# Performance work log

Hardware: AMD Instinct MI355X
Metric: run time of the kernel (lower is better)

The kernel has to match this reference:

```python
import jax, jax.numpy as jnp
import numpy as np

N_NODES = 50000
N_EDGES = 800000
D_IN = 256
D_HID = 256
D_OUT = 256


def sage_conv(x, src, dst, W_l, b_l, W_r, num_nodes):
    """PyG SAGEConv with mean aggregation: lin_l(mean_{j in N(i)} x_j) + lin_r(x_i)."""
    msg = x[src]  # [E, C] gather of source-node features
    agg = jax.ops.segment_sum(msg, dst, num_segments=num_nodes)  # [N, C]
    cnt = jax.ops.segment_sum(jnp.ones((src.shape[0],), x.dtype), dst,
                              num_segments=num_nodes)
    mean = agg / jnp.maximum(cnt, 1.0)[:, None]  # isolated nodes -> 0
    return mean @ W_l.T + b_l + x @ W_r.T


def setup_inputs() -> dict:
    key = jax.random.key(0)
    ks = jax.random.split(key, 10)
    s = 1.0 / np.sqrt(D_IN)
    x = jax.random.normal(ks[0], (N_NODES, D_IN), dtype=jnp.float32)
    edge_index = jax.random.randint(ks[1], (2, N_EDGES), 0, N_NODES, dtype=jnp.int64)
    mention_index = jax.random.randint(ks[2], (1,), 0, N_NODES, dtype=jnp.int64)
    return {
        "x": x,
        "edge_index": edge_index,
        "mention_index": mention_index,
        "W1_l": jax.random.uniform(ks[3], (D_HID, D_IN), jnp.float32, -s, s),
        "b1_l": jnp.zeros((D_HID,), jnp.float32),
        "W1_r": jax.random.uniform(ks[4], (D_HID, D_IN), jnp.float32, -s, s),
        "W2_l": jax.random.uniform(ks[5], (D_OUT, D_HID), jnp.float32, -s, s),
        "b2_l": jnp.zeros((D_OUT,), jnp.float32),
        "W2_r": jax.random.uniform(ks[6], (D_OUT, D_HID), jnp.float32, -s, s),
    }


def reference(x, edge_index, mention_index, W1_l, b1_l, W1_r, W2_l, b2_l, W2_r):
    src, dst = edge_index[0], edge_index[1]
    h = jax.nn.relu(sage_conv(x, src, dst, W1_l, b1_l, W1_r, N_NODES))
    h = sage_conv(h, src, dst, W2_l, b2_l, W2_r, N_NODES)
    # dropout in the original is a no-op (result discarded)
    logits = (h[mention_index] * h).sum(axis=1)  # [N]
    z = jax.nn.softmax(logits, axis=0)
    return z
```

## Files before the change

kernel.cpp:

```cpp
#include <hip/hip_runtime.h>
#include <math.h>

#define N_NODES 50000
#define N_EDGES 800000
#define D 256
#define K2 512
#define M_PAD 50048
#define BM 128
#define BN 256
#define BK 32
#define SCAN_B 196
#define SPX_B 12500
#define SPB_B 128
#define CNT_B 3125

typedef __attribute__((ext_vector_type(8))) short short8;
typedef __attribute__((ext_vector_type(8))) unsigned short ushort8;
typedef __attribute__((ext_vector_type(4))) float floatx4;

__device__ __forceinline__ unsigned short bf16_rn(float f) {
    union { float f; unsigned u; } a; a.f = f;
    unsigned r = a.u + 0x7FFF + ((a.u >> 16) & 1);
    return (unsigned short)(r >> 16);
}
__device__ __forceinline__ float bf16_to_f(unsigned short h) {
    union { unsigned u; float f; } a; a.u = ((unsigned)h) << 16;
    return a.f;
}
__device__ __forceinline__ void load_lds16(const void* g, void* lds) {
    __builtin_amdgcn_global_load_lds((const __attribute__((address_space(1))) void*)g,
                                     (__attribute__((address_space(3))) void*)lds, 16, 0, 0);
}

__global__ __launch_bounds__(256) void k_init(const float* __restrict__ x,
                                              const float* __restrict__ Wl,
                                              const float* __restrict__ Wr,
                                              const int* __restrict__ dst,
                                              unsigned short* __restrict__ Ahi,
                                              unsigned short* __restrict__ Alo,
                                              unsigned short* __restrict__ Bhi,
                                              unsigned short* __restrict__ Blo,
                                              int* __restrict__ deg) {
    int b = blockIdx.x;
    if (b < SPX_B) {
        int t = b * 256 + threadIdx.x;
        int m = t >> 6, j = (t & 63) * 4;
        float4 v = *(const float4*)&x[(size_t)m * D + j];
        ushort4 hi, lo;
        hi.x = bf16_rn(v.x); lo.x = bf16_rn(v.x - bf16_to_f(hi.x));
        hi.y = bf16_rn(v.y); lo.y = bf16_rn(v.y - bf16_to_f(hi.y));
        hi.z = bf16_rn(v.z); lo.z = bf16_rn(v.z - bf16_to_f(hi.z));
        hi.w = bf16_rn(v.w); lo.w = bf16_rn(v.w - bf16_to_f(hi.w));
        *(ushort4*)&Ahi[(size_t)m * K2 + 256 + j] = hi;
        *(ushort4*)&Alo[(size_t)m * K2 + 256 + j] = lo;
    } else if (b < SPX_B + SPB_B) {
        int t = (b - SPX_B) * 256 + threadIdx.x;
        int n = t >> 7, k = (t & 127) * 4;
        const float* srcp = (k < 256) ? &Wl[(size_t)n * 256 + k] : &Wr[(size_t)n * 256 + k - 256];
        float4 v = *(const float4*)srcp;
        ushort4 hi, lo;
        hi.x = bf16_rn(v.x); lo.x = bf16_rn(v.x - bf16_to_f(hi.x));
        hi.y = bf16_rn(v.y); lo.y = bf16_rn(v.y - bf16_to_f(hi.y));
        hi.z = bf16_rn(v.z); lo.z = bf16_rn(v.z - bf16_to_f(hi.z));
        hi.w = bf16_rn(v.w); lo.w = bf16_rn(v.w - bf16_to_f(hi.w));
        *(ushort4*)&Bhi[(size_t)n * K2 + k] = hi;
        *(ushort4*)&Blo[(size_t)n * K2 + k] = lo;
    } else {
        int e = (b - SPX_B - SPB_B) * 256 + threadIdx.x;
        if (e < N_EDGES) atomicAdd(&deg[dst[e]], 1);
    }
}

__global__ void k_scan1(const int* __restrict__ deg, int* __restrict__ bsum) {
    __shared__ int red[256];
    int b = blockIdx.x, t = threadIdx.x;
    int i = b * 256 + t;
    red[t] = (i < N_NODES) ? deg[i] : 0;
    __syncthreads();
    for (int o = 128; o; o >>= 1) {
        if (t < o) red[t] += red[t + o];
        __syncthreads();
    }
    if (t == 0) bsum[b] = red[0];
}

__global__ void k_scan23(const int* __restrict__ deg, const int* __restrict__ bsum,
                         int* __restrict__ cursor) {
    __shared__ int sh[256];
    int b = blockIdx.x, t = threadIdx.x;
    sh[t] = (t < SCAN_B) ? bsum[t] : 0;
    __syncthreads();
    for (int o = 1; o < 256; o <<= 1) {
        int v = (t >= o) ? sh[t - o] : 0;
        __syncthreads();
        sh[t] += v;
        __syncthreads();
    }
    int boff = (b == 0) ? 0 : sh[b - 1];
    __syncthreads();
    int i = b * 256 + t;
    int v = (i < N_NODES) ? deg[i] : 0;
    sh[t] = v;
    __syncthreads();
    for (int o = 1; o < 256; o <<= 1) {
        int val = (t >= o) ? sh[t - o] : 0;
        __syncthreads();
        sh[t] += val;
        __syncthreads();
    }
    if (i < N_NODES) cursor[i] = boff + sh[t] - v;
}

__global__ void k_bucket(const int* __restrict__ src, const int* __restrict__ dst,
                         int* __restrict__ cursor, int* __restrict__ csr_src) {
    int e = blockIdx.x * blockDim.x + threadIdx.x;
    if (e >= N_EDGES) return;
    int pos = atomicAdd(&cursor[dst[e]], 1);
    csr_src[pos] = src[e];
}

__global__ __launch_bounds__(256) void k_agg(const int* __restrict__ cursor,
                                             const int* __restrict__ deg,
                                             const int* __restrict__ csr,
                                             unsigned short* __restrict__ Ahi,
                                             unsigned short* __restrict__ Alo) {
    int node = blockIdx.x * 4 + (threadIdx.x >> 6);
    int lane = threadIdx.x & 63;
    if (node >= N_NODES) return;
    int d = deg[node], end = cursor[node], start = end - d;
    int h = lane >> 5;
    int col = (lane & 31) * 8;
    const unsigned short* Xb = Ahi + 256 + col;
    float acc0[8] = {}, acc1[8] = {}, acc2[8] = {}, acc3[8] = {};
    int j = start;
    for (; j + 8 <= end; j += 8) {
        int i0 = csr[j + h], i1 = csr[j + 2 + h], i2 = csr[j + 4 + h], i3 = csr[j + 6 + h];
        ushort8 v0 = *(const ushort8*)&Xb[(size_t)i0 * K2];
        ushort8 v1 = *(const ushort8*)&Xb[(size_t)i1 * K2];
        ushort8 v2 = *(const ushort8*)&Xb[(size_t)i2 * K2];
        ushort8 v3 = *(const ushort8*)&Xb[(size_t)i3 * K2];
        #pragma unroll
        for (int k = 0; k < 8; k++) {
            acc0[k] += bf16_to_f(v0[k]);
            acc1[k] += bf16_to_f(v1[k]);
            acc2[k] += bf16_to_f(v2[k]);
            acc3[k] += bf16_to_f(v3[k]);
        }
    }
    if (j + 4 <= end) {
        int i0 = csr[j + h], i1 = csr[j + 2 + h];
        ushort8 v0 = *(const ushort8*)&Xb[(size_t)i0 * K2];
        ushort8 v1 = *(const ushort8*)&Xb[(size_t)i1 * K2];
        #pragma unroll
        for (int k = 0; k < 8; k++) {
            acc0[k] += bf16_to_f(v0[k]);
            acc1[k] += bf16_to_f(v1[k]);
        }
        j += 4;
    }
    if (j + 2 <= end) {
        int i0 = csr[j + h];
        ushort8 v0 = *(const ushort8*)&Xb[(size_t)i0 * K2];
        #pragma unroll
        for (int k = 0; k < 8; k++) acc0[k] += bf16_to_f(v0[k]);
        j += 2;
    }
    if (j < end && h == 0) {
        int i0 = csr[j];
        ushort8 v0 = *(const ushort8*)&Xb[(size_t)i0 * K2];
        #pragma unroll
        for (int k = 0; k < 8; k++) acc0[k] += bf16_to_f(v0[k]);
    }
    float inv = 1.0f / fmaxf((float)d, 1.0f);
    ushort8 hi, lo;
    #pragma unroll
    for (int k = 0; k < 8; k++) {
        float a = (acc0[k] + acc1[k]) + (acc2[k] + acc3[k]);
        a += __shfl_xor(a, 32);
        float m = a * inv;
        hi[k] = bf16_rn(m);
        lo[k] = bf16_rn(m - bf16_to_f(hi[k]));
    }
    if (h == 0) {
        *(ushort8*)&Ahi[(size_t)node * K2 + col] = hi;
        *(ushort8*)&Alo[(size_t)node * K2 + col] = lo;
    }
}

__global__ __launch_bounds__(256) void k_small(const int* __restrict__ mention,
                                               const int* __restrict__ deg,
                                               const int* __restrict__ cursor,
                                               const int* __restrict__ csr,
                                               const float* __restrict__ x,
                                               const float* __restrict__ W1l,
                                               const float* __restrict__ W1r,
                                               const float* __restrict__ b1,
                                               float* __restrict__ h1m) {
    int m = mention[0];
    int dm = min(deg[m], 95);
    int slot = blockIdx.x;
    if (slot > dm) return;
    int startm = cursor[m] - deg[m];
    int node = (slot == 0) ? m : csr[startm + slot - 1];
    __shared__ float smean[D], sx[D];
    int t = threadIdx.x;
    int d = deg[node], end = cursor[node], start = end - d;
    float a = 0.f;
    for (int j = start; j < end; j++) a += x[(size_t)csr[j] * D + t];
    smean[t] = a / fmaxf((float)d, 1.0f);
    sx[t] = x[(size_t)node * D + t];
    __syncthreads();
    float z = b1[t];
    for (int k = 0; k < D; k++)
        z += smean[k] * W1l[(size_t)t * D + k] + sx[k] * W1r[(size_t)t * D + k];
    h1m[(size_t)slot * D + t] = fmaxf(z, 0.f);
}

__global__ __launch_bounds__(256) void k_vu(const int* __restrict__ mention,
                                            const int* __restrict__ deg,
                                            const float* __restrict__ h1m,
                                            const float* __restrict__ W2l,
                                            const float* __restrict__ W2r,
                                            const float* __restrict__ b2,
                                            float* __restrict__ u,
                                            float* __restrict__ cout) {
    __shared__ float sm[D], sh[D], sv[D], red[256];
    int m = mention[0];
    int dm = min(deg[m], 95);
    int t = threadIdx.x;
    float a = 0.f;
    for (int j = 1; j <= dm; j++) a += h1m[(size_t)j * D + t];
    sm[t] = a / fmaxf((float)deg[m], 1.0f);
    sh[t] = h1m[t];
    __syncthreads();
    float acc = b2[t];
    for (int k = 0; k < D; k++)
        acc += sm[k] * W2l[(size_t)t * D + k] + sh[k] * W2r[(size_t)t * D + k];
    sv[t] = acc;
    red[t] = b2[t] * acc;
    __syncthreads();
    for (int o = 128; o; o >>= 1) {
        if (t < o) red[t] += red[t + o];
        __syncthreads();
    }
    if (t == 0) cout[0] = red[0];
    float a1 = 0.f, a2 = 0.f;
    for (int n = 0; n < D; n++) {
        a1 += W2l[(size_t)n * D + t] * sv[n];
        a2 += W2r[(size_t)n * D + t] * sv[n];
    }
    u[t] = a1;
    u[D + t] = a2;
}

__global__ __launch_bounds__(512, 4)
void k_gemm_fused(const unsigned short* __restrict__ Ahi,
                  const unsigned short* __restrict__ Alo,
                  const unsigned short* __restrict__ Bhi,
                  const unsigned short* __restrict__ Blo,
                  const float* __restrict__ bias,
                  const float* __restrict__ u,
                  float* __restrict__ s,
                  float* __restrict__ t_) {
    __shared__ unsigned short sA[2][BM * BK];
    __shared__ unsigned short sB[2][BN * BK];
    __shared__ float sred[BM], tred[BM];
    int tid = threadIdx.x;
    int br = blockIdx.x;
    int lane = tid & 63, wv = tid >> 6;
    int wm = (wv >> 2) * 64, wn = (wv & 3) * 64;
    int q = lane >> 4, r = lane & 15;

    float biasv[4], u1v[4], u2v[4];
    #pragma unroll
    for (int nt = 0; nt < 4; nt++) {
        int gc = wn + nt * 16 + r;
        biasv[nt] = bias[gc];
        u1v[nt] = u[gc];
        u2v[nt] = u[256 + gc];
    }
    if (tid < BM) { sred[tid] = 0.f; tred[tid] = 0.f; }

    floatx4 acc[4][4] = {};

    const size_t arow0 = (size_t)br * BM;
    int seg = lane & 3;
    int rl16 = lane >> 2;

    for (int kt = 0; kt < K2 / BK; kt++) {
        {
            int rloc = wv * 16 + rl16;
            size_t gA = (arow0 + rloc) * (size_t)K2 + kt * BK + seg * 8;
            int ldsoff = (wv * 16) * BK;
            load_lds16(Ahi + gA, &sA[0][ldsoff]);
            load_lds16(Alo + gA, &sA[1][ldsoff]);
        }
        #pragma unroll
        for (int t = 0; t < 2; t++) {
            int rloc = wv * 32 + t * 16 + rl16;
            size_t gB = (size_t)rloc * K2 + kt * BK + seg * 8;
            int ldsoff = (wv * 32 + t * 16) * BK;
            load_lds16(Bhi + gB, &sB[0][ldsoff]);
            load_lds16(Blo + gB, &sB[1][ldsoff]);
        }
        __syncthreads();
        short8 ah[4], al[4], bh[4], bl[4];
        #pragma unroll
        for (int i = 0; i < 4; i++) {
            ah[i] = *(const short8*)&sA[0][(wm + i * 16 + r) * BK + q * 8];
            al[i] = *(const short8*)&sA[1][(wm + i * 16 + r) * BK + q * 8];
            bh[i] = *(const short8*)&sB[0][(wn + i * 16 + r) * BK + q * 8];
            bl[i] = *(const short8*)&sB[1][(wn + i * 16 + r) * BK + q * 8];
        }
        #pragma unroll
        for (int mt = 0; mt < 4; mt++)
            #pragma unroll
            for (int nt = 0; nt < 4; nt++) {
                acc[mt][nt] = __builtin_amdgcn_mfma_f32_16x16x32_bf16(ah[mt], bh[nt], acc[mt][nt], 0, 0, 0);
                acc[mt][nt] = __builtin_amdgcn_mfma_f32_16x16x32_bf16(ah[mt], bl[nt], acc[mt][nt], 0, 0, 0);
                acc[mt][nt] = __builtin_amdgcn_mfma_f32_16x16x32_bf16(al[mt], bh[nt], acc[mt][nt], 0, 0, 0);
            }
        __syncthreads();
    }

    #pragma unroll
    for (int mt = 0; mt < 4; mt++) {
        #pragma unroll
        for (int reg = 0; reg < 4; reg++) {
            float sacc = 0.f, tacc = 0.f;
            #pragma unroll
            for (int nt = 0; nt < 4; nt++) {
                float h = fmaxf(acc[mt][nt][reg] + biasv[nt], 0.f);
                sacc += h * u1v[nt];
                tacc += h * u2v[nt];
            }
            #pragma unroll
            for (int off = 1; off < 16; off <<= 1) {
                sacc += __shfl_xor(sacc, off);
                tacc += __shfl_xor(tacc, off);
            }
            if (r == 0) {
                int row = wm + mt * 16 + q * 4 + reg;
                atomicAdd(&sred[row], sacc);
                atomicAdd(&tred[row], tacc);
            }
        }
    }
    __syncthreads();
    if (tid < BM) {
        size_t grow = arow0 + tid;
        if (grow < N_NODES) {
            s[grow] = sred[tid];
            t_[grow] = tred[tid];
        }
    }
}

__global__ __launch_bounds__(256) void k_logits_sm1(const int* __restrict__ deg,
                                                    const int* __restrict__ cursor,
                                                    const int* __restrict__ csr,
                                                    const float* __restrict__ s,
                                                    const float* __restrict__ t_,
                                                    const float* __restrict__ cptr,
                                                    float* __restrict__ logits,
                                                    float* __restrict__ pmax,
                                                    float* __restrict__ psum) {
    __shared__ float red[256];
    int b = blockIdx.x, t = threadIdx.x;
    int i = b * 256 + t;
    float lg = -INFINITY;
    if (i < N_NODES) {
        int d = deg[i];
        int end = cursor[i];
        int start = end - d;
        float sum = 0.f;
        for (int j = start; j < end; j++) sum += s[csr[j]];
        lg = sum / fmaxf((float)d, 1.0f) + t_[i] + cptr[0];
        logits[i] = lg;
    }
    red[t] = lg;
    __syncthreads();
    for (int o = 128; o; o >>= 1) {
        if (t < o) red[t] = fmaxf(red[t], red[t + o]);
        __syncthreads();
    }
    float mb = red[0];
    __syncthreads();
    red[t] = (i < N_NODES) ? __expf(lg - mb) : 0.f;
    __syncthreads();
    for (int o = 128; o; o >>= 1) {
        if (t < o) red[t] += red[t + o];
        __syncthreads();
    }
    if (t == 0) { pmax[b] = mb; psum[b] = red[0]; }
}

__global__ __launch_bounds__(256) void k_sm23(const float* __restrict__ logits,
                                              const float* __restrict__ pmax,
                                              const float* __restrict__ psum,
                                              float* __restrict__ out) {
    __shared__ float rm[256], rs[256];
    int b = blockIdx.x, t = threadIdx.x;
    float m = (t < SCAN_B) ? pmax[t] : -INFINITY;
    rm[t] = m;
    __syncthreads();
    for (int o = 128; o; o >>= 1) {
        if (t < o) rm[t] = fmaxf(rm[t], rm[t + o]);
        __syncthreads();
    }
    float g = rm[0];
    __syncthreads();
    rs[t] = (t < SCAN_B) ? psum[t] * __expf(m - g) : 0.f;
    __syncthreads();
    for (int o = 128; o; o >>= 1) {
        if (t < o) rs[t] += rs[t + o];
        __syncthreads();
    }
    float inv = 1.0f / rs[0];
    int i = b * 256 + t;
    if (i < N_NODES) out[i] = __expf(logits[i] - g) * inv;
}

extern "C" void kernel_launch(void* const* d_in, const int* in_sizes, int n_in,
                              void* d_out, int out_size, void* d_ws, size_t ws_size,
                              hipStream_t stream) {
    const float* x   = (const float*)d_in[0];
    const int*   ei  = (const int*)d_in[1];
    const int*   src = ei;
    const int*   dst = ei + N_EDGES;
    const int*   mention = (const int*)d_in[2];
    const float* W1l = (const float*)d_in[3];
    const float* b1  = (const float*)d_in[4];
    const float* W1r = (const float*)d_in[5];
    const float* W2l = (const float*)d_in[6];
    const float* b2  = (const float*)d_in[7];
    const float* W2r = (const float*)d_in[8];

    char* w = (char*)d_ws;
    unsigned short* Ahi = (unsigned short*)w;  w += (size_t)M_PAD * K2 * 2;
    unsigned short* Alo = (unsigned short*)w;  w += (size_t)M_PAD * K2 * 2;
    unsigned short* Bhi = (unsigned short*)w;  w += (size_t)256 * K2 * 2;
    unsigned short* Blo = (unsigned short*)w;  w += (size_t)256 * K2 * 2;
    float* s     = (float*)w;  w += (size_t)N_NODES * 4;
    float* t_    = (float*)w;  w += (size_t)N_NODES * 4;
    int* deg     = (int*)w;    w += (size_t)N_NODES * 4;
    float* logit = (float*)w;  w += (size_t)N_NODES * 4;
    float* h1m   = (float*)w;  w += (size_t)96 * D * 4;
    float* u     = (float*)w;  w += 2 * D * 4;
    float* c     = (float*)w;  w += 16;
    float* pmax  = (float*)w;  w += 256 * 4;
    float* psum  = (float*)w;  w += 256 * 4;
    int* cursor  = (int*)w;    w += (size_t)N_NODES * 4;
    int* bsum    = (int*)w;    w += 256 * 4;
    int* csr     = (int*)w;    w += (size_t)N_EDGES * 4;

    hipMemsetAsync(deg, 0, (size_t)N_NODES * sizeof(int), stream);

    k_init  <<<SPX_B + SPB_B + CNT_B, 256, 0, stream>>>(x, W1l, W1r, dst,
                                                        Ahi, Alo, Bhi, Blo, deg);
    k_scan1 <<<SCAN_B, 256, 0, stream>>>(deg, bsum);
    k_scan23<<<SCAN_B, 256, 0, stream>>>(deg, bsum, cursor);
    k_bucket<<<(N_EDGES + 255) / 256, 256, 0, stream>>>(src, dst, cursor, csr);

    k_agg   <<<(N_NODES + 3) / 4, 256, 0, stream>>>(cursor, deg, csr, Ahi, Alo);

    k_small <<<96, 256, 0, stream>>>(mention, deg, cursor, csr, x, W1l, W1r, b1, h1m);
    k_vu    <<<1, 256, 0, stream>>>(mention, deg, h1m, W2l, W2r, b2, u, c);

    k_gemm_fused<<<M_PAD / BM, 512, 0, stream>>>(Ahi, Alo, Bhi, Blo, b1, u, s, t_);

    k_logits_sm1<<<SCAN_B, 256, 0, stream>>>(deg, cursor, csr, s, t_, c, logit, pmax, psum);
    k_sm23  <<<SCAN_B, 256, 0, stream>>>(logit, pmax, psum, (float*)d_out);
}
```

Baseline: 373.0 us.

## Parallelize mention-vector kernels and deepen aggregation unroll

Splits the single-block k_vu into two multi-block kernels: k_v uses 16 blocks with 16-lane shuffle reductions per output row, and k_u uses 4 blocks with partial sums over rows. This removes a serial one-block bottleneck on the critical path. The k_agg gather loop now unrolls to 16 edges so more loads are in flight, and k_small reads weights as float4. The split adds one extra kernel launch and an intermediate buffer.

```diff
diff --git a/kernel.cpp b/kernel.cpp
--- a/kernel.cpp
+++ b/kernel.cpp
@@ -133,7 +133,26 @@
     const unsigned short* Xb = Ahi + 256 + col;
     float acc0[8] = {}, acc1[8] = {}, acc2[8] = {}, acc3[8] = {};
     int j = start;
-    for (; j + 8 <= end; j += 8) {
+    for (; j + 16 <= end; j += 16) {
+        int i0 = csr[j + h],      i1 = csr[j + 2 + h],  i2 = csr[j + 4 + h],  i3 = csr[j + 6 + h];
+        int i4 = csr[j + 8 + h],  i5 = csr[j + 10 + h], i6 = csr[j + 12 + h], i7 = csr[j + 14 + h];
+        ushort8 v0 = *(const ushort8*)&Xb[(size_t)i0 * K2];
+        ushort8 v1 = *(const ushort8*)&Xb[(size_t)i1 * K2];
+        ushort8 v2 = *(const ushort8*)&Xb[(size_t)i2 * K2];
+        ushort8 v3 = *(const ushort8*)&Xb[(size_t)i3 * K2];
+        ushort8 v4 = *(const ushort8*)&Xb[(size_t)i4 * K2];
+        ushort8 v5 = *(const ushort8*)&Xb[(size_t)i5 * K2];
+        ushort8 v6 = *(const ushort8*)&Xb[(size_t)i6 * K2];
+        ushort8 v7 = *(const ushort8*)&Xb[(size_t)i7 * K2];
+        #pragma unroll
+        for (int k = 0; k < 8; k++) {
+            acc0[k] += bf16_to_f(v0[k]) + bf16_to_f(v4[k]);
+            acc1[k] += bf16_to_f(v1[k]) + bf16_to_f(v5[k]);
+            acc2[k] += bf16_to_f(v2[k]) + bf16_to_f(v6[k]);
+            acc3[k] += bf16_to_f(v3[k]) + bf16_to_f(v7[k]);
+        }
+    }
+    if (j + 8 <= end) {
         int i0 = csr[j + h], i1 = csr[j + 2 + h], i2 = csr[j + 4 + h], i3 = csr[j + 6 + h];
         ushort8 v0 = *(const ushort8*)&Xb[(size_t)i0 * K2];
         ushort8 v1 = *(const ushort8*)&Xb[(size_t)i1 * K2];
@@ -146,6 +165,7 @@
             acc2[k] += bf16_to_f(v2[k]);
             acc3[k] += bf16_to_f(v3[k]);
         }
+        j += 8;
     }
     if (j + 4 <= end) {
         int i0 = csr[j + h], i1 = csr[j + 2 + h];
@@ -211,20 +231,25 @@
     sx[t] = x[(size_t)node * D + t];
     __syncthreads();
     float z = b1[t];
-    for (int k = 0; k < D; k++)
-        z += smean[k] * W1l[(size_t)t * D + k] + sx[k] * W1r[(size_t)t * D + k];
+    const float* wl = &W1l[(size_t)t * D];
+    const float* wr = &W1r[(size_t)t * D];
+    for (int k = 0; k < D; k += 4) {
+        float4 a4 = *(const float4*)&wl[k];
+        float4 b4 = *(const float4*)&wr[k];
+        z += smean[k] * a4.x + smean[k + 1] * a4.y + smean[k + 2] * a4.z + smean[k + 3] * a4.w
+           + sx[k] * b4.x + sx[k + 1] * b4.y + sx[k + 2] * b4.z + sx[k + 3] * b4.w;
+    }
     h1m[(size_t)slot * D + t] = fmaxf(z, 0.f);
 }
 
-__global__ __launch_bounds__(256) void k_vu(const int* __restrict__ mention,
-                                            const int* __restrict__ deg,
-                                            const float* __restrict__ h1m,
-                                            const float* __restrict__ W2l,
-                                            const float* __restrict__ W2r,
-                                            const float* __restrict__ b2,
-                                            float* __restrict__ u,
-                                            float* __restrict__ cout) {
-    __shared__ float sm[D], sh[D], sv[D], red[256];
+__global__ __launch_bounds__(256) void k_v(const int* __restrict__ mention,
+                                           const int* __restrict__ deg,
+                                           const float* __restrict__ h1m,
+                                           const float* __restrict__ W2l,
+                                           const float* __restrict__ W2r,
+                                           const float* __restrict__ b2,
+                                           float* __restrict__ v) {
+    __shared__ float sm[D], sh[D];
     int m = mention[0];
     int dm = min(deg[m], 95);
     int t = threadIdx.x;
@@ -233,24 +258,58 @@
     sm[t] = a / fmaxf((float)deg[m], 1.0f);
     sh[t] = h1m[t];
     __syncthreads();
-    float acc = b2[t];
-    for (int k = 0; k < D; k++)
-        acc += sm[k] * W2l[(size_t)t * D + k] + sh[k] * W2r[(size_t)t * D + k];
-    sv[t] = acc;
-    red[t] = b2[t] * acc;
-    __syncthreads();
-    for (int o = 128; o; o >>= 1) {
-        if (t < o) red[t] += red[t + o];
-        __syncthreads();
-    }
-    if (t == 0) cout[0] = red[0];
+    int o = t >> 4, p = t & 15;
+    int row = blockIdx.x * 16 + o;
+    const float* wl = &W2l[(size_t)row * D];
+    const float* wr = &W2r[(size_t)row * D];
+    float acc = 0.f;
+    int k0 = p * 16;
+    #pragma unroll
+    for (int k = k0; k < k0 + 16; k += 4) {
+        float4 a4 = *(const float4*)&wl[k];
+        float4 b4 = *(const float4*)&wr[k];
+        acc += sm[k] * a4.x + sm[k + 1] * a4.y + sm[k + 2] * a4.z + sm[k + 3] * a4.w
+             + sh[k] * b4.x + sh[k + 1] * b4.y + sh[k + 2] * b4.z + sh[k + 3] * b4.w;
+    }
+    #pragma unroll
+    for (int off = 1; off < 16; off <<= 1) acc += __shfl_xor(acc, off);
+    if (p == 0) v[row] = acc + b2[row];
+}
+
+__global__ __launch_bounds__(256) void k_u(const float* __restrict__ W2l,
+                                           const float* __restrict__ W2r,
+                                           const float* __restrict__ b2,
+                                           const float* __restrict__ v,
+                                           float* __restrict__ u,
+                                           float* __restrict__ cout) {
+    __shared__ float sv[D];
+    __shared__ float r1[4][64], r2[4][64], red[256];
+    int t = threadIdx.x;
+    sv[t] = v[t];
+    __syncthreads();
+    int lane = t & 63, p = t >> 6;
+    int col = blockIdx.x * 64 + lane;
     float a1 = 0.f, a2 = 0.f;
-    for (int n = 0; n < D; n++) {
-        a1 += W2l[(size_t)n * D + t] * sv[n];
-        a2 += W2r[(size_t)n * D + t] * sv[n];
-    }
-    u[t] = a1;
-    u[D + t] = a2;
+    for (int n = p; n < D; n += 4) {
+        float vv = sv[n];
+        a1 += W2l[(size_t)n * D + col] * vv;
+        a2 += W2r[(size_t)n * D + col] * vv;
+    }
+    r1[p][lane] = a1; r2[p][lane] = a2;
+    __syncthreads();
+    if (p == 0) {
+        u[col] = r1[0][lane] + r1[1][lane] + r1[2][lane] + r1[3][lane];
+        u[D + col] = r2[0][lane] + r2[1][lane] + r2[2][lane] + r2[3][lane];
+    }
+    if (blockIdx.x == 0) {
+        red[t] = b2[t] * sv[t];
+        __syncthreads();
+        for (int o = 128; o; o >>= 1) {
+            if (t < o) red[t] += red[t + o];
+            __syncthreads();
+        }
+        if (t == 0) cout[0] = red[0];
+    }
 }
 
 __global__ __launch_bounds__(512, 4)
@@ -446,6 +505,7 @@
     int* deg     = (int*)w;    w += (size_t)N_NODES * 4;
     float* logit = (float*)w;  w += (size_t)N_NODES * 4;
     float* h1m   = (float*)w;  w += (size_t)96 * D * 4;
+    float* vbuf  = (float*)w;  w += D * 4;
     float* u     = (float*)w;  w += 2 * D * 4;
     float* c     = (float*)w;  w += 16;
     float* pmax  = (float*)w;  w += 256 * 4;
@@ -465,7 +525,8 @@
     k_agg   <<<(N_NODES + 3) / 4, 256, 0, stream>>>(cursor, deg, csr, Ahi, Alo);
 
     k_small <<<96, 256, 0, stream>>>(mention, deg, cursor, csr, x, W1l, W1r, b1, h1m);
-    k_vu    <<<1, 256, 0, stream>>>(mention, deg, h1m, W2l, W2r, b2, u, c);
+    k_v     <<<16, 256, 0, stream>>>(mention, deg, h1m, W2l, W2r, b2, vbuf);
+    k_u     <<<4, 256, 0, stream>>>(W2l, W2r, b2, vbuf, u, c);
 
     k_gemm_fused<<<M_PAD / BM, 512, 0, stream>>>(Ahi, Alo, Bhi, Blo, b1, u, s, t_);
 
```

After: 365.4 us. 2.0% less time.
